# Performance work log

Hardware: AMD Instinct MI355X
Metric: run time of the kernel (lower is better)

## Reference

```python
import jax, jax.numpy as jnp
import numpy as np

RATIO = 0.9375  # config.ratio


def setup_inputs() -> dict:
    key = jax.random.key(0)
    x = jax.random.normal(key, (4096, 8192), dtype=jnp.float32)
    return {"x": x}


def reference(x):
    # recall_window(x, ratio, dim=-1, keepdim=False)
    # For each row: sort, then find the minimum-length window covering
    # target = int(ratio * N) consecutive sorted values; return (left, right).
    N = x.shape[-1]
    target = int(RATIO * N)
    s = jnp.sort(x, axis=-1)                       # [R, N]
    # window_length[i] = s[i + target - 1] - s[i], for i in [0, N - target]
    lengths = s[:, target - 1:] - s[:, : N - target + 1]   # [R, N - target + 1]
    idx = jnp.argmin(lengths, axis=-1)             # first min, matches '<' in loop
    left = jnp.take_along_axis(s, idx[:, None], axis=-1)[:, 0]
    right = jnp.take_along_axis(s, (idx + target - 1)[:, None], axis=-1)[:, 0]
    return left, right
```

## Files before the change

### kernel.cpp

```cpp
#include <hip/hip_runtime.h>
#include <stdint.h>

#define ROWS   4096
#define NCOL   8192
#define TARGET 7680
#define NW     (NCOL - TARGET + 1)
#define NT     256
#define VPT    (NCOL / NT)
#define NB     2048
#define BPT    (NB / NT)
#define NWAVE  (NT / 64)
#define SCAP   2048
#define MAXS   (SCAP / NT)

struct Smem {
    uint32_t hist[NB];
    float    sorted[SCAP];
    float    sorted2[SCAP];
    uint32_t wsum[NWAVE];
    uint32_t res[4];
    float    fmin[NWAVE], fmax[NWAVE];
};

__device__ __forceinline__ int bin1f(float v, float mn, float s) {
    int b = (int)((v - mn) * s);
    return b > NB - 1 ? NB - 1 : b;
}
__device__ __forceinline__ int HIX(int b) { return ((b & 7) << 8) | (b >> 3); }

__global__ __launch_bounds__(NT, 4)
void recall_window_kernel(const float* __restrict__ x, float* __restrict__ out) {
    __shared__ Smem sm;
    const int tid = threadIdx.x;
    const int row = blockIdx.x;
    const int lane = tid & 63, wid = tid >> 6;

    float v[VPT];
    float mn = __int_as_float(0x7F800000), mx = -mn;
    const float4* xv = (const float4*)(x + (size_t)row * NCOL);
    #pragma unroll
    for (int j = 0; j < VPT / 4; j++) {
        float4 t = xv[tid + j * NT];
        v[4 * j + 0] = t.x; v[4 * j + 1] = t.y;
        v[4 * j + 2] = t.z; v[4 * j + 3] = t.w;
        mn = fminf(mn, fminf(fminf(t.x, t.y), fminf(t.z, t.w)));
        mx = fmaxf(mx, fmaxf(fmaxf(t.x, t.y), fmaxf(t.z, t.w)));
    }

    #pragma unroll
    for (int off = 32; off > 0; off >>= 1) {
        mn = fminf(mn, __shfl_down(mn, off, 64));
        mx = fmaxf(mx, __shfl_down(mx, off, 64));
    }
    if (lane == 0) { sm.fmin[wid] = mn; sm.fmax[wid] = mx; }
    #pragma unroll
    for (int j = 0; j < BPT; j++) sm.hist[tid + j * NT] = 0;
    __syncthreads();
    #pragma unroll
    for (int w = 0; w < NWAVE; w++) {
        mn = fminf(mn, sm.fmin[w]);
        mx = fmaxf(mx, sm.fmax[w]);
    }

    if (!(mx > mn)) {
        if (tid == 0) { out[row] = mn; out[ROWS + row] = mn; }
        return;
    }
    const float scale1 = (float)NB / (mx - mn);

    uint32_t binPk[VPT / 2];
    #pragma unroll
    for (int j = 0; j < VPT; j += 2) {
        int b0 = bin1f(v[j],     mn, scale1);
        int b1 = bin1f(v[j + 1], mn, scale1);
        binPk[j >> 1] = (uint32_t)b0 | ((uint32_t)b1 << 16);
        atomicAdd(&sm.hist[HIX(b0)], 1u);
        atomicAdd(&sm.hist[HIX(b1)], 1u);
    }
    __syncthreads();

    uint32_t h[BPT], s0 = 0;
    #pragma unroll
    for (int j = 0; j < BPT; j++) { h[j] = sm.hist[(j << 8) | tid]; s0 += h[j]; }
    uint32_t sc = s0;
    #pragma unroll
    for (int off = 1; off < 64; off <<= 1) {
        uint32_t n = __shfl_up(sc, off, 64);
        if (lane >= off) sc += n;
    }
    if (lane == 63) sm.wsum[wid] = sc;
    __syncthreads();
    uint32_t woff = 0;
    #pragma unroll
    for (int w = 0; w < NWAVE; w++) if (w < wid) woff += sm.wsum[w];
    const uint32_t incl = sc + woff, excl = incl - s0;
    const uint32_t ka = NW - 1, kb = TARGET - 1;
    if (ka >= excl && ka < incl) {
        uint32_t c = excl; bool done = false;
        #pragma unroll
        for (int j = 0; j < BPT; j++) {
            if (!done) {
                if (ka < c + h[j]) {
                    sm.res[0] = (uint32_t)(tid * BPT + j);
                    sm.res[1] = c + h[j];
                    done = true;
                } else c += h[j];
            }
        }
    }
    if (kb >= excl && kb < incl) {
        uint32_t c = excl; bool done = false;
        #pragma unroll
        for (int j = 0; j < BPT; j++) {
            if (!done) {
                if (kb < c + h[j]) {
                    sm.res[2] = (uint32_t)(tid * BPT + j);
                    sm.res[3] = c;
                    done = true;
                } else c += h[j];
            }
        }
    }
    {
        uint32_t run = excl;
        #pragma unroll
        for (int j = 0; j < BPT; j++) { sm.hist[(j << 8) | tid] = run; run += h[j]; }
    }
    __syncthreads();
    const int      B_lo    = (int)sm.res[0];
    const uint32_t cntB    = sm.res[1];
    const int      B_hi    = (int)sm.res[2];
    const uint32_t topBase = sm.res[3];
    const uint32_t shiftT  = cntB - topBase;
    uint32_t tot = cntB + (uint32_t)NCOL - topBase;
    if (tot > SCAP) tot = SCAP;

    #pragma unroll
    for (int j = 0; j < VPT; j++) {
        int b = (int)((binPk[j >> 1] >> ((j & 1) * 16)) & 0xffffu);
        if (b <= B_lo || b >= B_hi) {
            uint32_t pos = atomicAdd(&sm.hist[HIX(b)], 1u);
            if (b >= B_hi) pos += shiftT;
            if (pos < SCAP) sm.sorted[pos] = v[j];
        }
    }
    __syncthreads();

    #pragma unroll
    for (int it = 0; it < MAXS; it++) {
        int s = tid + it * NT;
        if (s < (int)tot) {
            float vv = sm.sorted[s];
            int b = bin1f(vv, mn, scale1);
            uint32_t en = sm.hist[HIX(b)];
            uint32_t st;
            if (s < (int)cntB) {
                st = (b == 0) ? 0u : sm.hist[HIX(b - 1)];
            } else {
                st = (b == B_hi) ? topBase : sm.hist[HIX(b - 1)];
                st += shiftT; en += shiftT;
            }
            if (en > tot) en = tot;
            uint32_t r = 0;
            if (en - st > 1) {
                for (uint32_t q = st; q < en; q++) {
                    float u = sm.sorted[q];
                    r += (u < vv) || (u == vv && (int)q < s);
                }
            }
            uint32_t d = st + r;
            if (d < SCAP) sm.sorted2[d] = vv;
        }
    }
    __syncthreads();


    if (wid == 0) {
        const int topstart = (int)tot - NW;
        float lbest = __int_as_float(0x7F800000);
        int   lidx  = 0x7FFFFFFF;
        for (int i = lane; i < NW; i += 64) {
            float len = sm.sorted2[topstart + i] - sm.sorted2[i];
            if (len < lbest) { lbest = len; lidx = i; }
        }
        #pragma unroll
        for (int off = 32; off > 0; off >>= 1) {
            float v2 = __shfl_down(lbest, off, 64);
            int   i2 = __shfl_down(lidx,  off, 64);
            if (v2 < lbest || (v2 == lbest && i2 < lidx)) { lbest = v2; lidx = i2; }
        }
        if (lane == 0) {
            out[row]        = sm.sorted2[lidx];
            out[ROWS + row] = sm.sorted2[topstart + lidx];
        }
    }
}

extern "C" void kernel_launch(void* const* d_in, const int* in_sizes, int n_in,
                              void* d_out, int out_size, void* d_ws, size_t ws_size,
                              hipStream_t stream) {
    const float* x = (const float*)d_in[0];
    float* out = (float*)d_out;
    recall_window_kernel<<<ROWS, NT, 0, stream>>>(x, out);
}
```

Baseline: 191.3 us.

## Use fixed-range histogram fast path and stop holding row values in registers

The first pass now bins values with a fixed range of [-4,4] clamped at both ends, so the min/max reduction and its barrier are skipped. If the candidate set overflows the shared buffer, it falls back to the old exact min/max path. Row values are no longer kept in registers; they are re-read from global memory (likely L2/L1 hits) for the scatter pass, which cuts VGPR pressure. The second sorted buffer is aliased onto the histogram through a union, with an extra barrier, to shrink LDS use. The fixed range is tuned to normally distributed inputs, but correctness is kept by the fallback.

New measurement: 217.7 us. 1.14x slower.

```diff
diff --git a/kernel.cpp b/kernel.cpp
--- a/kernel.cpp
+++ b/kernel.cpp
@@ -12,70 +12,38 @@
 #define NWAVE  (NT / 64)
 #define SCAP   2048
 #define MAXS   (SCAP / NT)
+#define FMN    (-4.0f)
+#define FSC    ((float)NB / 8.0f)
 
 struct Smem {
-    uint32_t hist[NB];
+    union {
+        uint32_t hist[NB];
+        float    sortedF[NB];
+    };
     float    sorted[SCAP];
-    float    sorted2[SCAP];
     uint32_t wsum[NWAVE];
     uint32_t res[4];
     float    fmin[NWAVE], fmax[NWAVE];
 };
 
-__device__ __forceinline__ int bin1f(float v, float mn, float s) {
+__device__ __forceinline__ int binf(float v, float mn, float s) {
     int b = (int)((v - mn) * s);
+    b = b < 0 ? 0 : b;
     return b > NB - 1 ? NB - 1 : b;
 }
 __device__ __forceinline__ int HIX(int b) { return ((b & 7) << 8) | (b >> 3); }
 
-__global__ __launch_bounds__(NT, 4)
-void recall_window_kernel(const float* __restrict__ x, float* __restrict__ out) {
-    __shared__ Smem sm;
-    const int tid = threadIdx.x;
-    const int row = blockIdx.x;
-    const int lane = tid & 63, wid = tid >> 6;
-
-    float v[VPT];
-    float mn = __int_as_float(0x7F800000), mx = -mn;
-    const float4* xv = (const float4*)(x + (size_t)row * NCOL);
-    #pragma unroll
-    for (int j = 0; j < VPT / 4; j++) {
-        float4 t = xv[tid + j * NT];
-        v[4 * j + 0] = t.x; v[4 * j + 1] = t.y;
-        v[4 * j + 2] = t.z; v[4 * j + 3] = t.w;
-        mn = fminf(mn, fminf(fminf(t.x, t.y), fminf(t.z, t.w)));
-        mx = fmaxf(mx, fmaxf(fmaxf(t.x, t.y), fmaxf(t.z, t.w)));
-    }
-
-    #pragma unroll
-    for (int off = 32; off > 0; off >>= 1) {
-        mn = fminf(mn, __shfl_down(mn, off, 64));
-        mx = fmaxf(mx, __shfl_down(mx, off, 64));
-    }
-    if (lane == 0) { sm.fmin[wid] = mn; sm.fmax[wid] = mx; }
-    #pragma unroll
-    for (int j = 0; j < BPT; j++) sm.hist[tid + j * NT] = 0;
-    __syncthreads();
-    #pragma unroll
-    for (int w = 0; w < NWAVE; w++) {
-        mn = fminf(mn, sm.fmin[w]);
-        mx = fmaxf(mx, sm.fmax[w]);
-    }
-
-    if (!(mx > mn)) {
-        if (tid == 0) { out[row] = mn; out[ROWS + row] = mn; }
-        return;
-    }
-    const float scale1 = (float)NB / (mx - mn);
-
-    uint32_t binPk[VPT / 2];
-    #pragma unroll
-    for (int j = 0; j < VPT; j += 2) {
-        int b0 = bin1f(v[j],     mn, scale1);
-        int b1 = bin1f(v[j + 1], mn, scale1);
-        binPk[j >> 1] = (uint32_t)b0 | ((uint32_t)b1 << 16);
-        atomicAdd(&sm.hist[HIX(b0)], 1u);
-        atomicAdd(&sm.hist[HIX(b1)], 1u);
+__device__ __forceinline__ bool do_row(Smem& sm, const float4* __restrict__ xv,
+                                       float amn, float asc, bool allow_fail,
+                                       float* __restrict__ out, int row,
+                                       int tid, int lane, int wid) {
+    #pragma unroll
+    for (int q = 0; q < VPT / 4; q++) {
+        float4 t = xv[tid + q * NT];
+        atomicAdd(&sm.hist[HIX(binf(t.x, amn, asc))], 1u);
+        atomicAdd(&sm.hist[HIX(binf(t.y, amn, asc))], 1u);
+        atomicAdd(&sm.hist[HIX(binf(t.z, amn, asc))], 1u);
+        atomicAdd(&sm.hist[HIX(binf(t.w, amn, asc))], 1u);
     }
     __syncthreads();
 
@@ -133,25 +101,34 @@
     const uint32_t topBase = sm.res[3];
     const uint32_t shiftT  = cntB - topBase;
     uint32_t tot = cntB + (uint32_t)NCOL - topBase;
+    if (allow_fail && tot > SCAP) return false;
     if (tot > SCAP) tot = SCAP;
 
     #pragma unroll
-    for (int j = 0; j < VPT; j++) {
-        int b = (int)((binPk[j >> 1] >> ((j & 1) * 16)) & 0xffffu);
-        if (b <= B_lo || b >= B_hi) {
-            uint32_t pos = atomicAdd(&sm.hist[HIX(b)], 1u);
-            if (b >= B_hi) pos += shiftT;
-            if (pos < SCAP) sm.sorted[pos] = v[j];
-        }
-    }
-    __syncthreads();
-
+    for (int q = 0; q < VPT / 4; q++) {
+        float4 t = xv[tid + q * NT];
+        #pragma unroll
+        for (int c4 = 0; c4 < 4; c4++) {
+            float val = c4 == 0 ? t.x : (c4 == 1 ? t.y : (c4 == 2 ? t.z : t.w));
+            int b = binf(val, amn, asc);
+            if (b <= B_lo || b >= B_hi) {
+                uint32_t pos = atomicAdd(&sm.hist[HIX(b)], 1u);
+                if (b >= B_hi) pos += shiftT;
+                if (pos < SCAP) sm.sorted[pos] = val;
+            }
+        }
+    }
+    __syncthreads();
+
+    float fvv[MAXS];
+    int   tgt[MAXS];
     #pragma unroll
     for (int it = 0; it < MAXS; it++) {
         int s = tid + it * NT;
+        tgt[it] = -1;
         if (s < (int)tot) {
             float vv = sm.sorted[s];
-            int b = bin1f(vv, mn, scale1);
+            int b = binf(vv, amn, asc);
             uint32_t en = sm.hist[HIX(b)];
             uint32_t st;
             if (s < (int)cntB) {
@@ -169,18 +146,21 @@
                 }
             }
             uint32_t d = st + r;
-            if (d < SCAP) sm.sorted2[d] = vv;
-        }
-    }
-    __syncthreads();
-
+            if (d < SCAP) { tgt[it] = (int)d; fvv[it] = vv; }
+        }
+    }
+    __syncthreads();
+    #pragma unroll
+    for (int it = 0; it < MAXS; it++)
+        if (tgt[it] >= 0) sm.sortedF[tgt[it]] = fvv[it];
+    __syncthreads();
 
     if (wid == 0) {
         const int topstart = (int)tot - NW;
         float lbest = __int_as_float(0x7F800000);
         int   lidx  = 0x7FFFFFFF;
         for (int i = lane; i < NW; i += 64) {
-            float len = sm.sorted2[topstart + i] - sm.sorted2[i];
+            float len = sm.sortedF[topstart + i] - sm.sortedF[i];
             if (len < lbest) { lbest = len; lidx = i; }
         }
         #pragma unroll
@@ -190,10 +170,60 @@
             if (v2 < lbest || (v2 == lbest && i2 < lidx)) { lbest = v2; lidx = i2; }
         }
         if (lane == 0) {
-            out[row]        = sm.sorted2[lidx];
-            out[ROWS + row] = sm.sorted2[topstart + lidx];
-        }
-    }
+            out[row]        = sm.sortedF[lidx];
+            out[ROWS + row] = sm.sortedF[topstart + lidx];
+        }
+    }
+    return true;
+}
+
+__global__ __launch_bounds__(NT, 4)
+void recall_window_kernel(const float* __restrict__ x, float* __restrict__ out) {
+    __shared__ Smem sm;
+    const int tid = threadIdx.x;
+    const int row = blockIdx.x;
+    const int lane = tid & 63, wid = tid >> 6;
+    const float4* xv = (const float4*)(x + (size_t)row * NCOL);
+
+    {
+        uint4 z; z.x = 0; z.y = 0; z.z = 0; z.w = 0;
+        *(uint4*)&sm.hist[tid * 4] = z;
+        *(uint4*)&sm.hist[NB / 2 + tid * 4] = z;
+    }
+    __syncthreads();
+
+    if (do_row(sm, xv, FMN, FSC, true, out, row, tid, lane, wid))
+        return;
+
+    float mn = __int_as_float(0x7F800000), mx = -mn;
+    #pragma unroll
+    for (int q = 0; q < VPT / 4; q++) {
+        float4 t = xv[tid + q * NT];
+        mn = fminf(mn, fminf(fminf(t.x, t.y), fminf(t.z, t.w)));
+        mx = fmaxf(mx, fmaxf(fmaxf(t.x, t.y), fmaxf(t.z, t.w)));
+    }
+    #pragma unroll
+    for (int off = 32; off > 0; off >>= 1) {
+        mn = fminf(mn, __shfl_down(mn, off, 64));
+        mx = fmaxf(mx, __shfl_down(mx, off, 64));
+    }
+    if (lane == 0) { sm.fmin[wid] = mn; sm.fmax[wid] = mx; }
+    {
+        uint4 z; z.x = 0; z.y = 0; z.z = 0; z.w = 0;
+        *(uint4*)&sm.hist[tid * 4] = z;
+        *(uint4*)&sm.hist[NB / 2 + tid * 4] = z;
+    }
+    __syncthreads();
+    #pragma unroll
+    for (int w = 0; w < NWAVE; w++) {
+        mn = fminf(mn, sm.fmin[w]);
+        mx = fmaxf(mx, sm.fmax[w]);
+    }
+    if (!(mx > mn)) {
+        if (tid == 0) { out[row] = mn; out[ROWS + row] = mn; }
+        return;
+    }
+    do_row(sm, xv, mn, (float)NB / (mx - mn), false, out, row, tid, lane, wid);
 }
 
 extern "C" void kernel_launch(void* const* d_in, const int* in_sizes, int n_in,
```

## Use single-wave blocks with fixed-threshold tail filtering and fallback path

Applied to the files above, without the earlier changes.

Rewrites the kernel to use one 64-lane wave per row and eliminate all block barriers. A fast path uses fixed thresholds (±1.38) to compact only tail values via ballot/popcount, then histograms, sorts and scans just those candidates with fixed bins. If the tail counts don't cover the window or overflow, it falls back to the data-dependent min/max histogram path, re-reading global memory instead of holding the row in registers. The fixed thresholds are tuned to the standard-normal test distribution, though correctness is preserved by the fallback.

Result: slower. 256.9 us (+34.3%).

```diff
diff --git a/kernel.cpp b/kernel.cpp
--- a/kernel.cpp
+++ b/kernel.cpp
@@ -5,153 +5,238 @@
 #define NCOL   8192
 #define TARGET 7680
 #define NW     (NCOL - TARGET + 1)
-#define NT     256
-#define VPT    (NCOL / NT)
+#define NT     64
+#define NF4    (NCOL / 4 / NT)
 #define NB     2048
-#define BPT    (NB / NT)
-#define NWAVE  (NT / 64)
-#define SCAP   2048
+#define BPL    (NB / NT)
+#define HALFB  (NB / 2)
+#define SCAP   1536
 #define MAXS   (SCAP / NT)
 
-struct Smem {
+#define T_LO   (-1.38f)
+#define T_HI   (1.38f)
+#define BMIN   (-4.0f)
+#define BSC    ((float)HALFB / (T_LO - BMIN))
+
+struct __align__(16) Smem {
     uint32_t hist[NB];
-    float    sorted[SCAP];
-    float    sorted2[SCAP];
-    uint32_t wsum[NWAVE];
-    uint32_t res[4];
-    float    fmin[NWAVE], fmax[NWAVE];
+    float    buf[SCAP];
 };
 
-__device__ __forceinline__ int bin1f(float v, float mn, float s) {
+__device__ __forceinline__ int HIX(int b) { return ((b & 31) << 6) | (b >> 5); }
+
+__device__ __forceinline__ int fbin(float v) {
+    if (v < T_LO) {
+        int b = (int)((v - BMIN) * BSC);
+        b = b < 0 ? 0 : b;
+        return b > HALFB - 1 ? HALFB - 1 : b;
+    }
+    int b = (int)((v - T_HI) * BSC);
+    b = b < 0 ? 0 : b;
+    b = b > HALFB - 1 ? HALFB - 1 : b;
+    return HALFB + b;
+}
+__device__ __forceinline__ int dbin(float v, float mn, float s) {
     int b = (int)((v - mn) * s);
+    b = b < 0 ? 0 : b;
     return b > NB - 1 ? NB - 1 : b;
 }
-__device__ __forceinline__ int HIX(int b) { return ((b & 7) << 8) | (b >> 3); }
 
 __global__ __launch_bounds__(NT, 4)
 void recall_window_kernel(const float* __restrict__ x, float* __restrict__ out) {
     __shared__ Smem sm;
-    const int tid = threadIdx.x;
-    const int row = blockIdx.x;
-    const int lane = tid & 63, wid = tid >> 6;
-
-    float v[VPT];
+    const int lane = threadIdx.x;
+    const int row  = blockIdx.x;
+    const float4* xv = (const float4*)(x + (size_t)row * NCOL);
+    const uint64_t below = (1ull << lane) - 1ull;
+
+    #pragma unroll
+    for (int j = 0; j < NB / 4 / NT; j++) {
+        uint4 z; z.x = 0; z.y = 0; z.z = 0; z.w = 0;
+        *(uint4*)&sm.hist[4 * (j * NT + lane)] = z;
+    }
+
+    uint32_t qc = 0, clo = 0, chi = 0;
+    #pragma unroll
+    for (int q = 0; q < NF4; q++) {
+        float4 t = xv[lane + q * NT];
+        #pragma unroll
+        for (int c = 0; c < 4; c++) {
+            float v = c == 0 ? t.x : c == 1 ? t.y : c == 2 ? t.z : t.w;
+            uint64_t mlo = __ballot(v < T_LO);
+            uint64_t mhi = __ballot(v > T_HI);
+            uint64_t m   = mlo | mhi;
+            if (m & (1ull << lane)) {
+                uint32_t off = qc + (uint32_t)__popcll(m & below);
+                if (off < SCAP) sm.buf[off] = v;
+            }
+            qc  += (uint32_t)__popcll(m);
+            clo += (uint32_t)__popcll(mlo);
+            chi += (uint32_t)__popcll(mhi);
+        }
+    }
+
+    if (clo >= NW && chi >= NW && qc <= SCAP) {
+        float qv[MAXS];
+        #pragma unroll
+        for (int it = 0; it < MAXS; it++) {
+            int s = lane + it * NT;
+            qv[it] = (s < (int)qc) ? sm.buf[s] : 0.f;
+        }
+        #pragma unroll
+        for (int it = 0; it < MAXS; it++) {
+            int s = lane + it * NT;
+            if (s < (int)qc) atomicAdd(&sm.hist[HIX(fbin(qv[it]))], 1u);
+        }
+        uint32_t h[BPL], s0 = 0;
+        #pragma unroll
+        for (int j = 0; j < BPL; j++) { h[j] = sm.hist[(j << 6) | lane]; s0 += h[j]; }
+        uint32_t sc = s0;
+        #pragma unroll
+        for (int off = 1; off < 64; off <<= 1) {
+            uint32_t n = __shfl_up(sc, off, 64);
+            if (lane >= off) sc += n;
+        }
+        uint32_t run = sc - s0;
+        #pragma unroll
+        for (int j = 0; j < BPL; j++) { sm.hist[(j << 6) | lane] = run; run += h[j]; }
+        #pragma unroll
+        for (int it = 0; it < MAXS; it++) {
+            int s = lane + it * NT;
+            if (s < (int)qc) {
+                int b = fbin(qv[it]);
+                uint32_t pos = atomicAdd(&sm.hist[HIX(b)], 1u);
+                sm.buf[pos] = qv[it];
+            }
+        }
+        float sv[MAXS]; int tg[MAXS];
+        #pragma unroll
+        for (int it = 0; it < MAXS; it++) {
+            int s = lane + it * NT; tg[it] = -1;
+            if (s < (int)qc) {
+                float vv = sm.buf[s];
+                int b = fbin(vv);
+                uint32_t en = sm.hist[HIX(b)];
+                uint32_t st = (b == 0) ? 0u : sm.hist[HIX(b - 1)];
+                uint32_t r = 0;
+                if (en - st > 1) {
+                    for (uint32_t p = st; p < en; p++) {
+                        float u = sm.buf[p];
+                        r += (u < vv) || (u == vv && (int)p < s);
+                    }
+                }
+                tg[it] = (int)(st + r); sv[it] = vv;
+            }
+        }
+        #pragma unroll
+        for (int it = 0; it < MAXS; it++)
+            if (tg[it] >= 0) sm.buf[tg[it]] = sv[it];
+
+        const int topstart = (int)qc - NW;
+        float lbest = __int_as_float(0x7F800000);
+        int   lidx  = 0x7FFFFFFF;
+        for (int i = lane; i < NW; i += NT) {
+            float len = sm.buf[topstart + i] - sm.buf[i];
+            if (len < lbest) { lbest = len; lidx = i; }
+        }
+        #pragma unroll
+        for (int off = 32; off > 0; off >>= 1) {
+            float v2 = __shfl_down(lbest, off, 64);
+            int   i2 = __shfl_down(lidx,  off, 64);
+            if (v2 < lbest || (v2 == lbest && i2 < lidx)) { lbest = v2; lidx = i2; }
+        }
+        if (lane == 0) {
+            out[row]        = sm.buf[lidx];
+            out[ROWS + row] = sm.buf[topstart + lidx];
+        }
+        return;
+    }
+
     float mn = __int_as_float(0x7F800000), mx = -mn;
-    const float4* xv = (const float4*)(x + (size_t)row * NCOL);
-    #pragma unroll
-    for (int j = 0; j < VPT / 4; j++) {
-        float4 t = xv[tid + j * NT];
-        v[4 * j + 0] = t.x; v[4 * j + 1] = t.y;
-        v[4 * j + 2] = t.z; v[4 * j + 3] = t.w;
+    #pragma unroll
+    for (int q = 0; q < NF4; q++) {
+        float4 t = xv[lane + q * NT];
         mn = fminf(mn, fminf(fminf(t.x, t.y), fminf(t.z, t.w)));
         mx = fmaxf(mx, fmaxf(fmaxf(t.x, t.y), fmaxf(t.z, t.w)));
     }
-
-    #pragma unroll
-    for (int off = 32; off > 0; off >>= 1) {
-        mn = fminf(mn, __shfl_down(mn, off, 64));
-        mx = fmaxf(mx, __shfl_down(mx, off, 64));
-    }
-    if (lane == 0) { sm.fmin[wid] = mn; sm.fmax[wid] = mx; }
-    #pragma unroll
-    for (int j = 0; j < BPT; j++) sm.hist[tid + j * NT] = 0;
-    __syncthreads();
-    #pragma unroll
-    for (int w = 0; w < NWAVE; w++) {
-        mn = fminf(mn, sm.fmin[w]);
-        mx = fmaxf(mx, sm.fmax[w]);
-    }
-
+    #pragma unroll
+    for (int off = 1; off < 64; off <<= 1) {
+        mn = fminf(mn, __shfl_xor(mn, off, 64));
+        mx = fmaxf(mx, __shfl_xor(mx, off, 64));
+    }
     if (!(mx > mn)) {
-        if (tid == 0) { out[row] = mn; out[ROWS + row] = mn; }
+        if (lane == 0) { out[row] = mn; out[ROWS + row] = mn; }
         return;
     }
-    const float scale1 = (float)NB / (mx - mn);
-
-    uint32_t binPk[VPT / 2];
-    #pragma unroll
-    for (int j = 0; j < VPT; j += 2) {
-        int b0 = bin1f(v[j],     mn, scale1);
-        int b1 = bin1f(v[j + 1], mn, scale1);
-        binPk[j >> 1] = (uint32_t)b0 | ((uint32_t)b1 << 16);
-        atomicAdd(&sm.hist[HIX(b0)], 1u);
-        atomicAdd(&sm.hist[HIX(b1)], 1u);
-    }
-    __syncthreads();
-
-    uint32_t h[BPT], s0 = 0;
-    #pragma unroll
-    for (int j = 0; j < BPT; j++) { h[j] = sm.hist[(j << 8) | tid]; s0 += h[j]; }
+    const float amn = mn, asc = (float)NB / (mx - mn);
+
+    #pragma unroll
+    for (int q = 0; q < NF4; q++) {
+        float4 t = xv[lane + q * NT];
+        atomicAdd(&sm.hist[HIX(dbin(t.x, amn, asc))], 1u);
+        atomicAdd(&sm.hist[HIX(dbin(t.y, amn, asc))], 1u);
+        atomicAdd(&sm.hist[HIX(dbin(t.z, amn, asc))], 1u);
+        atomicAdd(&sm.hist[HIX(dbin(t.w, amn, asc))], 1u);
+    }
+    uint32_t h[BPL], s0 = 0;
+    #pragma unroll
+    for (int j = 0; j < BPL; j++) { h[j] = sm.hist[(j << 6) | lane]; s0 += h[j]; }
     uint32_t sc = s0;
     #pragma unroll
     for (int off = 1; off < 64; off <<= 1) {
         uint32_t n = __shfl_up(sc, off, 64);
         if (lane >= off) sc += n;
     }
-    if (lane == 63) sm.wsum[wid] = sc;
-    __syncthreads();
-    uint32_t woff = 0;
-    #pragma unroll
-    for (int w = 0; w < NWAVE; w++) if (w < wid) woff += sm.wsum[w];
-    const uint32_t incl = sc + woff, excl = incl - s0;
+    const uint32_t excl = sc - s0;
     const uint32_t ka = NW - 1, kb = TARGET - 1;
-    if (ka >= excl && ka < incl) {
-        uint32_t c = excl; bool done = false;
-        #pragma unroll
-        for (int j = 0; j < BPT; j++) {
-            if (!done) {
-                if (ka < c + h[j]) {
-                    sm.res[0] = (uint32_t)(tid * BPT + j);
-                    sm.res[1] = c + h[j];
-                    done = true;
-                } else c += h[j];
-            }
-        }
-    }
-    if (kb >= excl && kb < incl) {
-        uint32_t c = excl; bool done = false;
-        #pragma unroll
-        for (int j = 0; j < BPT; j++) {
-            if (!done) {
-                if (kb < c + h[j]) {
-                    sm.res[2] = (uint32_t)(tid * BPT + j);
-                    sm.res[3] = c;
-                    done = true;
-                } else c += h[j];
-            }
-        }
-    }
+    uint32_t encA = 0xFFFFFFFFu, encB = 0xFFFFFFFFu;
     {
-        uint32_t run = excl;
-        #pragma unroll
-        for (int j = 0; j < BPT; j++) { sm.hist[(j << 8) | tid] = run; run += h[j]; }
-    }
-    __syncthreads();
-    const int      B_lo    = (int)sm.res[0];
-    const uint32_t cntB    = sm.res[1];
-    const int      B_hi    = (int)sm.res[2];
-    const uint32_t topBase = sm.res[3];
+        uint32_t c = excl;
+        #pragma unroll
+        for (int j = 0; j < BPL; j++) {
+            if (ka >= c && ka < c + h[j]) encA = ((uint32_t)(lane * BPL + j) << 14) | (c + h[j]);
+            if (kb >= c && kb < c + h[j]) encB = ((uint32_t)(lane * BPL + j) << 14) | c;
+            c += h[j];
+        }
+    }
+    #pragma unroll
+    for (int off = 1; off < 64; off <<= 1) {
+        uint32_t a2 = __shfl_xor(encA, off, 64); encA = a2 < encA ? a2 : encA;
+        uint32_t b2 = __shfl_xor(encB, off, 64); encB = b2 < encB ? b2 : encB;
+    }
+    const int      B_lo    = (int)(encA >> 14);
+    const uint32_t cntB    = encA & 0x3FFFu;
+    const int      B_hi    = (int)(encB >> 14);
+    const uint32_t topBase = encB & 0x3FFFu;
     const uint32_t shiftT  = cntB - topBase;
     uint32_t tot = cntB + (uint32_t)NCOL - topBase;
     if (tot > SCAP) tot = SCAP;
-
-    #pragma unroll
-    for (int j = 0; j < VPT; j++) {
-        int b = (int)((binPk[j >> 1] >> ((j & 1) * 16)) & 0xffffu);
-        if (b <= B_lo || b >= B_hi) {
-            uint32_t pos = atomicAdd(&sm.hist[HIX(b)], 1u);
-            if (b >= B_hi) pos += shiftT;
-            if (pos < SCAP) sm.sorted[pos] = v[j];
-        }
-    }
-    __syncthreads();
-
+    {
+        uint32_t run = excl;
+        #pragma unroll
+        for (int j = 0; j < BPL; j++) { sm.hist[(j << 6) | lane] = run; run += h[j]; }
+    }
+    #pragma unroll
+    for (int q = 0; q < NF4; q++) {
+        float4 t = xv[lane + q * NT];
+        #pragma unroll
+        for (int c = 0; c < 4; c++) {
+            float v = c == 0 ? t.x : c == 1 ? t.y : c == 2 ? t.z : t.w;
+            int b = dbin(v, amn, asc);
+            if (b <= B_lo || b >= B_hi) {
+                uint32_t pos = atomicAdd(&sm.hist[HIX(b)], 1u);
+                if (b >= B_hi) pos += shiftT;
+                if (pos < SCAP) sm.buf[pos] = v;
+            }
+        }
+    }
+    float sv[MAXS]; int tg[MAXS];
     #pragma unroll
     for (int it = 0; it < MAXS; it++) {
-        int s = tid + it * NT;
+        int s = lane + it * NT; tg[it] = -1;
         if (s < (int)tot) {
-            float vv = sm.sorted[s];
-            int b = bin1f(vv, mn, scale1);
+            float vv = sm.buf[s];
+            int b = dbin(vv, amn, asc);
             uint32_t en = sm.hist[HIX(b)];
             uint32_t st;
             if (s < (int)cntB) {
@@ -163,36 +248,35 @@
             if (en > tot) en = tot;
             uint32_t r = 0;
             if (en - st > 1) {
-                for (uint32_t q = st; q < en; q++) {
-                    float u = sm.sorted[q];
-                    r += (u < vv) || (u == vv && (int)q < s);
+                for (uint32_t p = st; p < en; p++) {
+                    float u = sm.buf[p];
+                    r += (u < vv) || (u == vv && (int)p < s);
                 }
             }
             uint32_t d = st + r;
-            if (d < SCAP) sm.sorted2[d] = vv;
-        }
-    }
-    __syncthreads();
-
-
-    if (wid == 0) {
-        const int topstart = (int)tot - NW;
-        float lbest = __int_as_float(0x7F800000);
-        int   lidx  = 0x7FFFFFFF;
-        for (int i = lane; i < NW; i += 64) {
-            float len = sm.sorted2[topstart + i] - sm.sorted2[i];
-            if (len < lbest) { lbest = len; lidx = i; }
-        }
-        #pragma unroll
-        for (int off = 32; off > 0; off >>= 1) {
-            float v2 = __shfl_down(lbest, off, 64);
-            int   i2 = __shfl_down(lidx,  off, 64);
-            if (v2 < lbest || (v2 == lbest && i2 < lidx)) { lbest = v2; lidx = i2; }
-        }
-        if (lane == 0) {
-            out[row]        = sm.sorted2[lidx];
-            out[ROWS + row] = sm.sorted2[topstart + lidx];
-        }
+            if (d < SCAP) { tg[it] = (int)d; sv[it] = vv; }
+        }
+    }
+    #pragma unroll
+    for (int it = 0; it < MAXS; it++)
+        if (tg[it] >= 0) sm.buf[tg[it]] = sv[it];
+
+    const int topstart = (int)tot - NW;
+    float lbest = __int_as_float(0x7F800000);
+    int   lidx  = 0x7FFFFFFF;
+    for (int i = lane; i < NW; i += NT) {
+        float len = sm.buf[topstart + i] - sm.buf[i];
+        if (len < lbest) { lbest = len; lidx = i; }
+    }
+    #pragma unroll
+    for (int off = 32; off > 0; off >>= 1) {
+        float v2 = __shfl_down(lbest, off, 64);
+        int   i2 = __shfl_down(lidx,  off, 64);
+        if (v2 < lbest || (v2 == lbest && i2 < lidx)) { lbest = v2; lidx = i2; }
+    }
+    if (lane == 0) {
+        out[row]        = sm.buf[lidx];
+        out[ROWS + row] = sm.buf[topstart + lidx];
     }
 }
 
```
